# Performance work log

Measured on AMD Instinct MI355X. Metric: run time of the kernel, lower is better.

## Reference

```python
import jax, jax.numpy as jnp
import numpy as np

N_CELLS = 19683   # 27**3 lattice
K = 26            # Moore-neighborhood max_neighbors
D = 128           # state_size
HG = 64           # gating hidden
CNF_STEPS = 3     # integration_steps
DT = 0.1


def setup_inputs() -> dict:
    key = jax.random.key(0)
    ks = jax.random.split(key, 12)
    s = lambda fan_in: 1.0 / np.sqrt(fan_in)
    return {
        "current_state": jax.random.normal(ks[0], (N_CELLS, D), jnp.float32),
        "neighbor_states": jax.random.normal(ks[1], (N_CELLS, K, D), jnp.float32),
        "conn_type": jax.random.randint(ks[2], (N_CELLS, K), 0, 3, jnp.int32),
        "W_local": jax.random.normal(ks[3], (2 * D, D), jnp.float32) * s(2 * D),
        "b_local": jnp.zeros((D,), jnp.float32),
        "W_msg": jax.random.normal(ks[4], (2 * D, D), jnp.float32) * s(2 * D),
        "b_msg": jnp.zeros((D,), jnp.float32),
        "W_upd": jax.random.normal(ks[5], (2 * D, D), jnp.float32) * s(2 * D),
        "b_upd": jnp.zeros((D,), jnp.float32),
        "W_cnf": jax.random.normal(ks[6], (2 * D, D), jnp.float32) * s(2 * D),
        "b_cnf": jnp.zeros((D,), jnp.float32),
        "W_g1": jax.random.normal(ks[7], (D, HG), jnp.float32) * s(D),
        "b_g1": jnp.zeros((HG,), jnp.float32),
        "W_g2": jax.random.normal(ks[8], (HG, 3), jnp.float32) * s(HG),
        "b_g2": jnp.zeros((3,), jnp.float32),
    }


def _masked_mean(nbr, mask):
    # nbr: [N,K,D], mask: [N,K] float -> [N,D]
    cnt = jnp.maximum(mask.sum(-1, keepdims=True), 1.0)
    return jnp.einsum("nkd,nk->nd", nbr, mask) / cnt


def reference(current_state, neighbor_states, conn_type,
              W_local, b_local, W_msg, b_msg, W_upd, b_upd,
              W_cnf, b_cnf, W_g1, b_g1, W_g2, b_g2):
    cur = current_state                       # [N,D]
    nbr = neighbor_states                     # [N,K,D]
    m_l = (conn_type == 0).astype(cur.dtype)  # local mask   [N,K]
    m_f = (conn_type == 1).astype(cur.dtype)  # functional
    m_d = (conn_type == 2).astype(cur.dtype)  # distant

    # --- local expert: SimpleLinear over [cell, mean(local neighbors)] ---
    agg_l = _masked_mean(nbr, m_l)
    local_out = jnp.tanh(jnp.concatenate([cur, agg_l], -1) @ W_local + b_local)

    # --- functional expert: GNN message passing ---
    cur_b = jnp.broadcast_to(cur[:, None, :], nbr.shape)          # [N,K,D]
    edge_in = jnp.concatenate([cur_b, nbr], -1)                   # [N,K,2D]
    msgs = jax.nn.relu(edge_in @ W_msg + b_msg)                   # [N,K,D]
    agg_msg = _masked_mean(msgs, m_f)                             # [N,D]
    func_out = jnp.tanh(jnp.concatenate([cur, agg_msg], -1) @ W_upd + b_upd)

    # --- distant expert: lightweight CNF (fixed-step Euler) ---
    agg_d = _masked_mean(nbr, m_d)

    def euler_step(s, _):
        ds = jnp.tanh(jnp.concatenate([s, agg_d], -1) @ W_cnf + b_cnf)
        return s + DT * ds, None

    distant_out, _ = jax.lax.scan(euler_step, cur, None, length=CNF_STEPS)

    # --- gating network: softmax over 3 experts ---
    gates = jax.nn.softmax(jax.nn.relu(cur @ W_g1 + b_g1) @ W_g2 + b_g2, -1)  # [N,3]

    out = (gates[:, 0:1] * local_out
           + gates[:, 1:2] * func_out
           + gates[:, 2:3] * distant_out)
    return out
```

## Files before the change

### kernel.cpp

```cpp
#include <hip/hip_runtime.h>
#include <hip/hip_bf16.h>
#include <math.h>

#define NC 19683
#define KN 26
#define DD 128
#define HGN 64
#define LDSB 136
#define DTC 0.1f

using bf8v = __attribute__((ext_vector_type(8))) short;
using f4v  = __attribute__((ext_vector_type(4))) float;

__device__ __forceinline__ unsigned short f2bf(float x) {
    union { float f; unsigned u; } v; v.f = x;
    unsigned r = v.u + 0x7fffu + ((v.u >> 16) & 1u);
    return (unsigned short)(r >> 16);
}

__global__ __launch_bounds__(256) void k_prep(const float* __restrict__ Wl,
    const float* __restrict__ Wm, const float* __restrict__ Wu,
    const float* __restrict__ Wc, unsigned short* __restrict__ WT)
{
    int idx = blockIdx.x * 256 + threadIdx.x;
    int m = idx >> 15;
    int r = idx & 32767;
    int j = r >> 8;
    int i = r & 255;
    const float* src = (m == 0) ? Wl : (m == 1) ? Wm : (m == 2) ? Wu : Wc;
    WT[idx] = f2bf(src[i * DD + j]);
}

__global__ __launch_bounds__(256) void kA(const float* __restrict__ cur,
    const unsigned short* __restrict__ WT, const float* __restrict__ b_msg,
    const float* __restrict__ Wg1, const float* __restrict__ bg1,
    const float* __restrict__ Wg2, const float* __restrict__ bg2,
    float* __restrict__ P, float* __restrict__ gates)
{
    __shared__ __align__(16) unsigned short Al[32][LDSB];
    __shared__ __align__(16) unsigned short Bl[128][LDSB];
    __shared__ float curf[32][DD];
    __shared__ float hrelu[32][HGN];
    int t = threadIdx.x;
    int n0 = blockIdx.x * 32;

    for (int p = 0; p < 16; ++p) {
        int idx = p * 256 + t;
        int r = idx >> 7, c = idx & 127;
        float v = (n0 + r < NC) ? cur[(size_t)(n0 + r) * DD + c] : 0.f;
        curf[r][c] = v;
        Al[r][c] = f2bf(v);
    }
    const unsigned short* WmT = WT + 1 * 32768;
    for (int p = 0; p < 8; ++p) {
        int ch = p * 256 + t;
        int j = ch >> 4, i8 = (ch & 15) * 8;
        *(bf8v*)&Bl[j][i8] = *(const bf8v*)&WmT[j * 256 + i8];
    }
    __syncthreads();

    int w = t >> 6, lane = t & 63;
    int mt = w & 1, colh = w >> 1;
    int lm = lane & 15, lq = lane >> 4;
    for (int nt = 0; nt < 4; ++nt) {
        int col0 = colh * 64 + nt * 16;
        f4v acc = {0.f, 0.f, 0.f, 0.f};
        for (int s = 0; s < 4; ++s) {
            bf8v a = *(const bf8v*)&Al[mt * 16 + lm][s * 32 + lq * 8];
            bf8v b = *(const bf8v*)&Bl[col0 + lm][s * 32 + lq * 8];
            acc = __builtin_amdgcn_mfma_f32_16x16x32_bf16(a, b, acc, 0, 0, 0);
        }
        int col = col0 + lm;
        float bm = b_msg[col];
        for (int r = 0; r < 4; ++r) {
            int row = mt * 16 + lq * 4 + r;
            int n = n0 + row;
            if (n < NC) P[(size_t)n * DD + col] = acc[r] + bm;
        }
    }

    for (int p = 0; p < 8; ++p) {
        int idx = p * 256 + t;
        int c = idx >> 6, g = idx & 63;
        float s = bg1[g];
        for (int i = 0; i < DD; ++i) s += curf[c][i] * Wg1[i * HGN + g];
        hrelu[c][g] = fmaxf(s, 0.f);
    }
    __syncthreads();
    if (t < 32) {
        int n = n0 + t;
        if (n < NC) {
            float l[3];
            for (int e = 0; e < 3; ++e) {
                float s = bg2[e];
                for (int g = 0; g < HGN; ++g) s += hrelu[t][g] * Wg2[g * 3 + e];
                l[e] = s;
            }
            float m = fmaxf(l[0], fmaxf(l[1], l[2]));
            float e0 = expf(l[0] - m), e1 = expf(l[1] - m), e2 = expf(l[2] - m);
            float inv = 1.f / (e0 + e1 + e2);
            gates[n * 4 + 0] = e0 * inv;
            gates[n * 4 + 1] = e1 * inv;
            gates[n * 4 + 2] = e2 * inv;
        }
    }
}

__global__ __launch_bounds__(256) void kB(const float* __restrict__ nbr,
    const int* __restrict__ conn, const unsigned short* __restrict__ WT,
    const float* __restrict__ P, float* __restrict__ agg_l,
    float* __restrict__ agg_m, float* __restrict__ agg_d)
{
    __shared__ __align__(16) unsigned short Bl[128][LDSB];
    __shared__ __align__(16) unsigned short Al[2][32][LDSB];
    __shared__ float pbuf[2][DD];
    __shared__ float mlm[2][32], mfm[2][32], mdm[2][32];
    __shared__ float icnt[2][4];
    int t = threadIdx.x;
    int n0 = blockIdx.x * 2;

    if (t < 64) {
        int c = t >> 5, k = t & 31;
        float vl = 0.f, vf = 0.f, vd = 0.f;
        if (k < KN && n0 + c < NC) {
            int ct = conn[(size_t)(n0 + c) * KN + k];
            vl = (ct == 0) ? 1.f : 0.f;
            vf = (ct == 1) ? 1.f : 0.f;
            vd = (ct == 2) ? 1.f : 0.f;
        }
        mlm[c][k] = vl; mfm[c][k] = vf; mdm[c][k] = vd;
    }
    {
        int c = t >> 7, j = t & 127;
        pbuf[c][j] = (n0 + c < NC) ? P[(size_t)(n0 + c) * DD + j] : 0.f;
    }
    const unsigned short* Wm2T = WT + 32768 + 128;
    for (int p = 0; p < 8; ++p) {
        int ch = p * 256 + t;
        int j = ch >> 4, i8 = (ch & 15) * 8;
        *(bf8v*)&Bl[j][i8] = *(const bf8v*)&Wm2T[j * 256 + i8];
    }
    __syncthreads();

    if (t < 2) {
        float cl = 0.f, cf = 0.f, cd = 0.f;
        for (int k = 0; k < KN; ++k) { cl += mlm[t][k]; cf += mfm[t][k]; cd += mdm[t][k]; }
        icnt[t][0] = 1.f / fmaxf(cl, 1.f);
        icnt[t][1] = 1.f / fmaxf(cf, 1.f);
        icnt[t][2] = 1.f / fmaxf(cd, 1.f);
    }

    int c = t >> 7, j = t & 127;
    float sl = 0.f, sd = 0.f;
    if (n0 + c < NC) {
        const float* base = nbr + (size_t)(n0 + c) * KN * DD + j;
        #pragma unroll
        for (int k = 0; k < KN; ++k) {
            float v = base[(size_t)k * DD];
            sl += mlm[c][k] * v;
            sd += mdm[c][k] * v;
            Al[c][k][j] = f2bf(v);
        }
    } else {
        for (int k = 0; k < KN; ++k) Al[c][k][j] = 0;
    }
    for (int k = KN; k < 32; ++k) Al[c][k][j] = 0;
    __syncthreads();

    if (n0 + c < NC) {
        agg_l[(size_t)(n0 + c) * DD + j] = sl * icnt[c][0];
        agg_d[(size_t)(n0 + c) * DD + j] = sd * icnt[c][2];
    }

    int w = t >> 6, lane = t & 63;
    int cc = w >> 1, colh = w & 1;
    int lm = lane & 15, lq = lane >> 4;
    if (n0 + cc < NC) {
        float icf = icnt[cc][1];
        for (int nt = 0; nt < 4; ++nt) {
            int col0 = colh * 64 + nt * 16;
            float pv = pbuf[cc][col0 + lm];
            float msum = 0.f;
            for (int mtile = 0; mtile < 2; ++mtile) {
                f4v acc = {0.f, 0.f, 0.f, 0.f};
                for (int s = 0; s < 4; ++s) {
                    bf8v a = *(const bf8v*)&Al[cc][mtile * 16 + lm][s * 32 + lq * 8];
                    bf8v b = *(const bf8v*)&Bl[col0 + lm][s * 32 + lq * 8];
                    acc = __builtin_amdgcn_mfma_f32_16x16x32_bf16(a, b, acc, 0, 0, 0);
                }
                for (int r = 0; r < 4; ++r) {
                    int row = mtile * 16 + lq * 4 + r;
                    if (mfm[cc][row] > 0.f) msum += fmaxf(pv + acc[r], 0.f);
                }
            }
            msum += __shfl_xor(msum, 16, 64);
            msum += __shfl_xor(msum, 32, 64);
            if (lane < 16) agg_m[(size_t)(n0 + cc) * DD + col0 + lane] = msum * icf;
        }
    }
}

__global__ __launch_bounds__(256) void kC(const float* __restrict__ cur,
    const unsigned short* __restrict__ WT, const float* __restrict__ agg_l,
    const float* __restrict__ agg_m, const float* __restrict__ agg_d,
    const float* __restrict__ b_local, const float* __restrict__ b_upd,
    const float* __restrict__ b_cnf, const float* __restrict__ gates,
    float* __restrict__ out)
{
    __shared__ __align__(16) unsigned short Wl[128][LDSB];
    __shared__ __align__(16) unsigned short Xc[32][LDSB];
    __shared__ __align__(16) unsigned short Xa[32][LDSB];
    __shared__ float glds[32][4];
    __shared__ float bl[DD], bu[DD], bc[DD];
    int t = threadIdx.x;
    int n0 = blockIdx.x * 32;
    int w = t >> 6, lane = t & 63;
    int mt = w & 1, colh = w >> 1;
    int lm = lane & 15, lq = lane >> 4;

    auto stageW = [&](int m, int koff) {
        const unsigned short* src = WT + m * 32768 + koff;
        for (int p = 0; p < 8; ++p) {
            int ch = p * 256 + t;
            int j = ch >> 4, i8 = (ch & 15) * 8;
            *(bf8v*)&Wl[j][i8] = *(const bf8v*)&src[j * 256 + i8];
        }
    };
    auto stageXa = [&](const float* src) {
        for (int p = 0; p < 16; ++p) {
            int idx = p * 256 + t;
            int r = idx >> 7, ccol = idx & 127;
            float v = (n0 + r < NC) ? src[(size_t)(n0 + r) * DD + ccol] : 0.f;
            Xa[r][ccol] = f2bf(v);
        }
    };
    auto mfmaPass = [&](unsigned short (&X)[32][LDSB], f4v* acc) {
        for (int nt = 0; nt < 4; ++nt) {
            int col0 = colh * 64 + nt * 16;
            for (int s = 0; s < 4; ++s) {
                bf8v a = *(const bf8v*)&X[mt * 16 + lm][s * 32 + lq * 8];
                bf8v b = *(const bf8v*)&Wl[col0 + lm][s * 32 + lq * 8];
                acc[nt] = __builtin_amdgcn_mfma_f32_16x16x32_bf16(a, b, acc[nt], 0, 0, 0);
            }
        }
    };

    for (int p = 0; p < 16; ++p) {
        int idx = p * 256 + t;
        int r = idx >> 7, ccol = idx & 127;
        float v = (n0 + r < NC) ? cur[(size_t)(n0 + r) * DD + ccol] : 0.f;
        Xc[r][ccol] = f2bf(v);
    }
    if (t < 128) { bl[t] = b_local[t]; bu[t] = b_upd[t]; bc[t] = b_cnf[t]; }
    if (t >= 128 && t < 160) {
        int r = t - 128; int n = n0 + r;
        float g0 = 0.f, g1 = 0.f, g2 = 0.f;
        if (n < NC) { g0 = gates[n * 4]; g1 = gates[n * 4 + 1]; g2 = gates[n * 4 + 2]; }
        glds[r][0] = g0; glds[r][1] = g1; glds[r][2] = g2;
    }
    stageW(0, 0);
    __syncthreads();

    f4v oacc[4], acc[4];
    for (int nt = 0; nt < 4; ++nt) oacc[nt] = (f4v){0.f, 0.f, 0.f, 0.f};

    for (int nt = 0; nt < 4; ++nt) acc[nt] = (f4v){0.f, 0.f, 0.f, 0.f};
    mfmaPass(Xc, acc);
    __syncthreads();
    stageW(0, 128); stageXa(agg_l);
    __syncthreads();
    mfmaPass(Xa, acc);
    for (int nt = 0; nt < 4; ++nt) {
        int col = colh * 64 + nt * 16 + lm;
        for (int r = 0; r < 4; ++r) {
            int row = mt * 16 + lq * 4 + r;
            oacc[nt][r] += glds[row][0] * tanhf(acc[nt][r] + bl[col]);
        }
    }

    __syncthreads();
    stageW(2, 0);
    __syncthreads();
    for (int nt = 0; nt < 4; ++nt) acc[nt] = (f4v){0.f, 0.f, 0.f, 0.f};
    mfmaPass(Xc, acc);
    __syncthreads();
    stageW(2, 128); stageXa(agg_m);
    __syncthreads();
    mfmaPass(Xa, acc);
    for (int nt = 0; nt < 4; ++nt) {
        int col = colh * 64 + nt * 16 + lm;
        for (int r = 0; r < 4; ++r) {
            int row = mt * 16 + lq * 4 + r;
            oacc[nt][r] += glds[row][1] * tanhf(acc[nt][r] + bu[col]);
        }
    }

    __syncthreads();
    stageW(3, 128); stageXa(agg_d);
    __syncthreads();
    for (int nt = 0; nt < 4; ++nt) acc[nt] = (f4v){0.f, 0.f, 0.f, 0.f};
    mfmaPass(Xa, acc);
    f4v hd[4], s[4];
    for (int nt = 0; nt < 4; ++nt) {
        int col = colh * 64 + nt * 16 + lm;
        for (int r = 0; r < 4; ++r) {
            int row = mt * 16 + lq * 4 + r;
            int n = n0 + row;
            hd[nt][r] = acc[nt][r] + bc[col];
            s[nt][r] = (n < NC) ? cur[(size_t)n * DD + col] : 0.f;
        }
    }
    __syncthreads();
    stageW(3, 0);
    for (int step = 0; step < 3; ++step) {
        for (int nt = 0; nt < 4; ++nt) {
            int col = colh * 64 + nt * 16 + lm;
            for (int r = 0; r < 4; ++r) {
                int row = mt * 16 + lq * 4 + r;
                Xa[row][col] = f2bf(s[nt][r]);
            }
        }
        __syncthreads();
        for (int nt = 0; nt < 4; ++nt) acc[nt] = (f4v){0.f, 0.f, 0.f, 0.f};
        mfmaPass(Xa, acc);
        for (int nt = 0; nt < 4; ++nt)
            for (int r = 0; r < 4; ++r)
                s[nt][r] += DTC * tanhf(acc[nt][r] + hd[nt][r]);
        __syncthreads();
    }

    for (int nt = 0; nt < 4; ++nt) {
        int col = colh * 64 + nt * 16 + lm;
        for (int r = 0; r < 4; ++r) {
            int row = mt * 16 + lq * 4 + r;
            int n = n0 + row;
            if (n < NC) out[(size_t)n * DD + col] = oacc[nt][r] + glds[row][2] * s[nt][r];
        }
    }
}

extern "C" void kernel_launch(void* const* d_in, const int* in_sizes, int n_in,
                              void* d_out, int out_size, void* d_ws, size_t ws_size,
                              hipStream_t stream) {
    const float* cur     = (const float*)d_in[0];
    const float* nbr     = (const float*)d_in[1];
    const int*   conn    = (const int*)d_in[2];
    const float* W_local = (const float*)d_in[3];
    const float* b_local = (const float*)d_in[4];
    const float* W_msg   = (const float*)d_in[5];
    const float* b_msg   = (const float*)d_in[6];
    const float* W_upd   = (const float*)d_in[7];
    const float* b_upd   = (const float*)d_in[8];
    const float* W_cnf   = (const float*)d_in[9];
    const float* b_cnf   = (const float*)d_in[10];
    const float* Wg1     = (const float*)d_in[11];
    const float* bg1     = (const float*)d_in[12];
    const float* Wg2     = (const float*)d_in[13];
    const float* bg2     = (const float*)d_in[14];
    float* out = (float*)d_out;

    char* ws = (char*)d_ws;
    unsigned short* WT = (unsigned short*)ws;
    float* P     = (float*)(ws + 262144);
    float* gatesb = (float*)(ws + 262144 + 10077696);
    float* aggl  = (float*)(ws + 262144 + 10077696 + 314928);
    float* aggm  = aggl + (size_t)NC * DD;
    float* aggd  = aggm + (size_t)NC * DD;

    hipLaunchKernelGGL(k_prep, dim3(512), dim3(256), 0, stream, W_local, W_msg, W_upd, W_cnf, WT);
    hipLaunchKernelGGL(kA, dim3(616), dim3(256), 0, stream, cur, WT, b_msg, Wg1, bg1, Wg2, bg2, P, gatesb);
    hipLaunchKernelGGL(kB, dim3(9842), dim3(256), 0, stream, nbr, conn, WT, P, aggl, aggm, aggd);
    hipLaunchKernelGGL(kC, dim3(616), dim3(256), 0, stream, cur, WT, aggl, aggm, aggd, b_local, b_upd, b_cnf, gatesb, out);
}
```

Measured before the change: 544.2 us.

## Restructure neighbor kernel per-wave, store aggregates as bf16, MFMA gating

The neighbor kernel now assigns one cell per wave (four cells per block). It builds the connection-type masks with wave ballots and popcounts instead of shared-memory arrays, and uses float2 vector loads for the neighbor rows. The three aggregate buffers are written as bf16 instead of fp32, which halves the intermediate traffic between the neighbor kernel and the final kernel, and the final kernel reads them with 16-byte vector loads. The gating first layer moves from a scalar fp32 loop to bf16 MFMA using a pre-transposed weight, which gives up some precision in the gates and the aggregates.

```diff
diff --git a/kernel.cpp b/kernel.cpp
--- a/kernel.cpp
+++ b/kernel.cpp
@@ -17,74 +17,98 @@
     unsigned r = v.u + 0x7fffu + ((v.u >> 16) & 1u);
     return (unsigned short)(r >> 16);
 }
+__device__ __forceinline__ unsigned pk2(float a, float b) {
+    return ((unsigned)f2bf(a)) | (((unsigned)f2bf(b)) << 16);
+}
 
 __global__ __launch_bounds__(256) void k_prep(const float* __restrict__ Wl,
     const float* __restrict__ Wm, const float* __restrict__ Wu,
-    const float* __restrict__ Wc, unsigned short* __restrict__ WT)
+    const float* __restrict__ Wc, const float* __restrict__ Wg1,
+    unsigned short* __restrict__ WT, unsigned short* __restrict__ WgT)
 {
     int idx = blockIdx.x * 256 + threadIdx.x;
-    int m = idx >> 15;
-    int r = idx & 32767;
-    int j = r >> 8;
-    int i = r & 255;
-    const float* src = (m == 0) ? Wl : (m == 1) ? Wm : (m == 2) ? Wu : Wc;
-    WT[idx] = f2bf(src[i * DD + j]);
+    if (idx < 131072) {
+        int m = idx >> 15;
+        int r = idx & 32767;
+        int j = r >> 8;
+        int i = r & 255;
+        const float* src = (m == 0) ? Wl : (m == 1) ? Wm : (m == 2) ? Wu : Wc;
+        WT[idx] = f2bf(src[i * DD + j]);
+    } else {
+        int idx2 = idx - 131072;
+        int col = idx2 >> 7;
+        int k = idx2 & 127;
+        WgT[idx2] = f2bf(Wg1[k * HGN + col]);
+    }
 }
 
 __global__ __launch_bounds__(256) void kA(const float* __restrict__ cur,
-    const unsigned short* __restrict__ WT, const float* __restrict__ b_msg,
-    const float* __restrict__ Wg1, const float* __restrict__ bg1,
+    const unsigned short* __restrict__ WT, const unsigned short* __restrict__ WgT,
+    const float* __restrict__ b_msg, const float* __restrict__ bg1,
     const float* __restrict__ Wg2, const float* __restrict__ bg2,
     float* __restrict__ P, float* __restrict__ gates)
 {
     __shared__ __align__(16) unsigned short Al[32][LDSB];
     __shared__ __align__(16) unsigned short Bl[128][LDSB];
-    __shared__ float curf[32][DD];
-    __shared__ float hrelu[32][HGN];
+    __shared__ __align__(16) unsigned short Gl[64][LDSB];
+    __shared__ float hrelu[32][HGN + 4];
     int t = threadIdx.x;
     int n0 = blockIdx.x * 32;
-
-    for (int p = 0; p < 16; ++p) {
+    int w = t >> 6, lane = t & 63;
+    int lm = lane & 15, lq = lane >> 4;
+
+    for (int p = 0; p < 8; ++p) {
         int idx = p * 256 + t;
-        int r = idx >> 7, c = idx & 127;
-        float v = (n0 + r < NC) ? cur[(size_t)(n0 + r) * DD + c] : 0.f;
-        curf[r][c] = v;
-        Al[r][c] = f2bf(v);
-    }
-    const unsigned short* WmT = WT + 1 * 32768;
+        int r = idx >> 6, c2 = (idx & 63) * 2;
+        float2 v = {0.f, 0.f};
+        if (n0 + r < NC) v = *(const float2*)&cur[(size_t)(n0 + r) * DD + c2];
+        *(unsigned*)&Al[r][c2] = pk2(v.x, v.y);
+    }
+    const unsigned short* WmT = WT + 32768;
     for (int p = 0; p < 8; ++p) {
         int ch = p * 256 + t;
         int j = ch >> 4, i8 = (ch & 15) * 8;
         *(bf8v*)&Bl[j][i8] = *(const bf8v*)&WmT[j * 256 + i8];
     }
-    __syncthreads();
-
-    int w = t >> 6, lane = t & 63;
-    int mt = w & 1, colh = w >> 1;
-    int lm = lane & 15, lq = lane >> 4;
-    for (int nt = 0; nt < 4; ++nt) {
-        int col0 = colh * 64 + nt * 16;
-        f4v acc = {0.f, 0.f, 0.f, 0.f};
-        for (int s = 0; s < 4; ++s) {
-            bf8v a = *(const bf8v*)&Al[mt * 16 + lm][s * 32 + lq * 8];
-            bf8v b = *(const bf8v*)&Bl[col0 + lm][s * 32 + lq * 8];
-            acc = __builtin_amdgcn_mfma_f32_16x16x32_bf16(a, b, acc, 0, 0, 0);
-        }
-        int col = col0 + lm;
-        float bm = b_msg[col];
-        for (int r = 0; r < 4; ++r) {
-            int row = mt * 16 + lq * 4 + r;
-            int n = n0 + row;
-            if (n < NC) P[(size_t)n * DD + col] = acc[r] + bm;
-        }
-    }
-
-    for (int p = 0; p < 8; ++p) {
-        int idx = p * 256 + t;
-        int c = idx >> 6, g = idx & 63;
-        float s = bg1[g];
-        for (int i = 0; i < DD; ++i) s += curf[c][i] * Wg1[i * HGN + g];
-        hrelu[c][g] = fmaxf(s, 0.f);
+    for (int p = 0; p < 4; ++p) {
+        int ch = p * 256 + t;
+        int j = ch >> 4, i8 = (ch & 15) * 8;
+        *(bf8v*)&Gl[j][i8] = *(const bf8v*)&WgT[j * 128 + i8];
+    }
+    __syncthreads();
+
+    {
+        int mt = w & 1, colh = w >> 1;
+        for (int nt = 0; nt < 4; ++nt) {
+            int col0 = colh * 64 + nt * 16;
+            f4v acc = {0.f, 0.f, 0.f, 0.f};
+            for (int s = 0; s < 4; ++s) {
+                bf8v a = *(const bf8v*)&Al[mt * 16 + lm][s * 32 + lq * 8];
+                bf8v b = *(const bf8v*)&Bl[col0 + lm][s * 32 + lq * 8];
+                acc = __builtin_amdgcn_mfma_f32_16x16x32_bf16(a, b, acc, 0, 0, 0);
+            }
+            int col = col0 + lm;
+            float bm = b_msg[col];
+            for (int r = 0; r < 4; ++r) {
+                int row = mt * 16 + lq * 4 + r;
+                int n = n0 + row;
+                if (n < NC) P[(size_t)n * DD + col] = acc[r] + bm;
+            }
+        }
+    }
+    {
+        int col0 = w * 16;
+        float bg = bg1[col0 + lm];
+        for (int mt2 = 0; mt2 < 2; ++mt2) {
+            f4v acc = {0.f, 0.f, 0.f, 0.f};
+            for (int s = 0; s < 4; ++s) {
+                bf8v a = *(const bf8v*)&Al[mt2 * 16 + lm][s * 32 + lq * 8];
+                bf8v b = *(const bf8v*)&Gl[col0 + lm][s * 32 + lq * 8];
+                acc = __builtin_amdgcn_mfma_f32_16x16x32_bf16(a, b, acc, 0, 0, 0);
+            }
+            for (int r = 0; r < 4; ++r)
+                hrelu[mt2 * 16 + lq * 4 + r][col0 + lm] = fmaxf(acc[r] + bg, 0.f);
+        }
     }
     __syncthreads();
     if (t < 32) {
@@ -108,101 +132,95 @@
 
 __global__ __launch_bounds__(256) void kB(const float* __restrict__ nbr,
     const int* __restrict__ conn, const unsigned short* __restrict__ WT,
-    const float* __restrict__ P, float* __restrict__ agg_l,
-    float* __restrict__ agg_m, float* __restrict__ agg_d)
+    const float* __restrict__ P, unsigned short* __restrict__ agg_l,
+    unsigned short* __restrict__ agg_m, unsigned short* __restrict__ agg_d)
 {
     __shared__ __align__(16) unsigned short Bl[128][LDSB];
-    __shared__ __align__(16) unsigned short Al[2][32][LDSB];
-    __shared__ float pbuf[2][DD];
-    __shared__ float mlm[2][32], mfm[2][32], mdm[2][32];
-    __shared__ float icnt[2][4];
+    __shared__ __align__(16) unsigned short Al[4][32][LDSB];
+    __shared__ float P8[4][DD];
     int t = threadIdx.x;
-    int n0 = blockIdx.x * 2;
-
-    if (t < 64) {
-        int c = t >> 5, k = t & 31;
-        float vl = 0.f, vf = 0.f, vd = 0.f;
-        if (k < KN && n0 + c < NC) {
-            int ct = conn[(size_t)(n0 + c) * KN + k];
-            vl = (ct == 0) ? 1.f : 0.f;
-            vf = (ct == 1) ? 1.f : 0.f;
-            vd = (ct == 2) ? 1.f : 0.f;
-        }
-        mlm[c][k] = vl; mfm[c][k] = vf; mdm[c][k] = vd;
-    }
-    {
-        int c = t >> 7, j = t & 127;
-        pbuf[c][j] = (n0 + c < NC) ? P[(size_t)(n0 + c) * DD + j] : 0.f;
-    }
+    int n0 = blockIdx.x * 4;
+    int w = t >> 6, lane = t & 63;
+    int n = n0 + w;
+    bool act = n < NC;
+
     const unsigned short* Wm2T = WT + 32768 + 128;
     for (int p = 0; p < 8; ++p) {
         int ch = p * 256 + t;
         int j = ch >> 4, i8 = (ch & 15) * 8;
         *(bf8v*)&Bl[j][i8] = *(const bf8v*)&Wm2T[j * 256 + i8];
     }
-    __syncthreads();
-
-    if (t < 2) {
-        float cl = 0.f, cf = 0.f, cd = 0.f;
-        for (int k = 0; k < KN; ++k) { cl += mlm[t][k]; cf += mfm[t][k]; cd += mdm[t][k]; }
-        icnt[t][0] = 1.f / fmaxf(cl, 1.f);
-        icnt[t][1] = 1.f / fmaxf(cf, 1.f);
-        icnt[t][2] = 1.f / fmaxf(cd, 1.f);
-    }
-
-    int c = t >> 7, j = t & 127;
-    float sl = 0.f, sd = 0.f;
-    if (n0 + c < NC) {
-        const float* base = nbr + (size_t)(n0 + c) * KN * DD + j;
-        #pragma unroll
-        for (int k = 0; k < KN; ++k) {
-            float v = base[(size_t)k * DD];
-            sl += mlm[c][k] * v;
-            sd += mdm[c][k] * v;
-            Al[c][k][j] = f2bf(v);
-        }
-    } else {
-        for (int k = 0; k < KN; ++k) Al[c][k][j] = 0;
-    }
-    for (int k = KN; k < 32; ++k) Al[c][k][j] = 0;
-    __syncthreads();
-
-    if (n0 + c < NC) {
-        agg_l[(size_t)(n0 + c) * DD + j] = sl * icnt[c][0];
-        agg_d[(size_t)(n0 + c) * DD + j] = sd * icnt[c][2];
-    }
-
-    int w = t >> 6, lane = t & 63;
-    int cc = w >> 1, colh = w & 1;
-    int lm = lane & 15, lq = lane >> 4;
-    if (n0 + cc < NC) {
-        float icf = icnt[cc][1];
-        for (int nt = 0; nt < 4; ++nt) {
-            int col0 = colh * 64 + nt * 16;
-            float pv = pbuf[cc][col0 + lm];
+    {
+        int idx = t * 2;
+        int r = idx >> 7, c = idx & 127;
+        float2 v = {0.f, 0.f};
+        if (n0 + r < NC) v = *(const float2*)&P[(size_t)(n0 + r) * DD + c];
+        *(float2*)&P8[r][c] = v;
+    }
+    int ct = 3;
+    if (act && lane < KN) ct = conn[(size_t)n * KN + lane];
+    unsigned long long mlb = __ballot(ct == 0);
+    unsigned long long mfb = __ballot(ct == 1);
+    unsigned long long mdb = __ballot(ct == 2);
+    float icl = 1.f / fmaxf((float)__builtin_popcountll(mlb), 1.f);
+    float icf = 1.f / fmaxf((float)__builtin_popcountll(mfb), 1.f);
+    float icd = 1.f / fmaxf((float)__builtin_popcountll(mdb), 1.f);
+
+    int j2 = lane * 2;
+    const float* base = nbr + ((size_t)(act ? n : 0) * KN) * DD + j2;
+    float2 vv[KN];
+    #pragma unroll
+    for (int k = 0; k < KN; ++k) {
+        float2 v = {0.f, 0.f};
+        if (act) v = *(const float2*)&base[(size_t)k * DD];
+        vv[k] = v;
+    }
+    float slx = 0.f, sly = 0.f, sdx = 0.f, sdy = 0.f;
+    #pragma unroll
+    for (int k = 0; k < KN; ++k) {
+        float2 v = vv[k];
+        if ((mlb >> k) & 1) { slx += v.x; sly += v.y; }
+        if ((mdb >> k) & 1) { sdx += v.x; sdy += v.y; }
+        *(unsigned*)&Al[w][k][j2] = pk2(v.x, v.y);
+    }
+    {
+        unsigned* pz = (unsigned*)&Al[w][KN][0];
+        for (int z = lane; z < (32 - KN) * LDSB / 2; z += 64) pz[z] = 0;
+    }
+    if (act) {
+        *(unsigned*)&agg_l[(size_t)n * DD + j2] = pk2(slx * icl, sly * icl);
+        *(unsigned*)&agg_d[(size_t)n * DD + j2] = pk2(sdx * icd, sdy * icd);
+    }
+    __syncthreads();
+
+    if (act) {
+        int lm = lane & 15, lq = lane >> 4;
+        for (int nt = 0; nt < 8; ++nt) {
+            int col0 = nt * 16;
+            float pv = P8[w][col0 + lm];
             float msum = 0.f;
-            for (int mtile = 0; mtile < 2; ++mtile) {
+            for (int mt2 = 0; mt2 < 2; ++mt2) {
                 f4v acc = {0.f, 0.f, 0.f, 0.f};
                 for (int s = 0; s < 4; ++s) {
-                    bf8v a = *(const bf8v*)&Al[cc][mtile * 16 + lm][s * 32 + lq * 8];
+                    bf8v a = *(const bf8v*)&Al[w][mt2 * 16 + lm][s * 32 + lq * 8];
                     bf8v b = *(const bf8v*)&Bl[col0 + lm][s * 32 + lq * 8];
                     acc = __builtin_amdgcn_mfma_f32_16x16x32_bf16(a, b, acc, 0, 0, 0);
                 }
                 for (int r = 0; r < 4; ++r) {
-                    int row = mtile * 16 + lq * 4 + r;
-                    if (mfm[cc][row] > 0.f) msum += fmaxf(pv + acc[r], 0.f);
+                    int row = mt2 * 16 + lq * 4 + r;
+                    if ((mfb >> row) & 1) msum += fmaxf(pv + acc[r], 0.f);
                 }
             }
             msum += __shfl_xor(msum, 16, 64);
             msum += __shfl_xor(msum, 32, 64);
-            if (lane < 16) agg_m[(size_t)(n0 + cc) * DD + col0 + lane] = msum * icf;
+            if (lane < 16) agg_m[(size_t)n * DD + col0 + lane] = f2bf(msum * icf);
         }
     }
 }
 
 __global__ __launch_bounds__(256) void kC(const float* __restrict__ cur,
-    const unsigned short* __restrict__ WT, const float* __restrict__ agg_l,
-    const float* __restrict__ agg_m, const float* __restrict__ agg_d,
+    const unsigned short* __restrict__ WT, const unsigned short* __restrict__ agg_l,
+    const unsigned short* __restrict__ agg_m, const unsigned short* __restrict__ agg_d,
     const float* __restrict__ b_local, const float* __restrict__ b_upd,
     const float* __restrict__ b_cnf, const float* __restrict__ gates,
     float* __restrict__ out)
@@ -226,12 +244,13 @@
             *(bf8v*)&Wl[j][i8] = *(const bf8v*)&src[j * 256 + i8];
         }
     };
-    auto stageXa = [&](const float* src) {
-        for (int p = 0; p < 16; ++p) {
+    auto stageXa = [&](const unsigned short* src) {
+        for (int p = 0; p < 2; ++p) {
             int idx = p * 256 + t;
-            int r = idx >> 7, ccol = idx & 127;
-            float v = (n0 + r < NC) ? src[(size_t)(n0 + r) * DD + ccol] : 0.f;
-            Xa[r][ccol] = f2bf(v);
+            int r = idx >> 4, c8 = (idx & 15) * 8;
+            bf8v v = {0, 0, 0, 0, 0, 0, 0, 0};
+            if (n0 + r < NC) v = *(const bf8v*)&src[(size_t)(n0 + r) * DD + c8];
+            *(bf8v*)&Xa[r][c8] = v;
         }
     };
     auto mfmaPass = [&](unsigned short (&X)[32][LDSB], f4v* acc) {
@@ -245,11 +264,12 @@
         }
     };
 
-    for (int p = 0; p < 16; ++p) {
+    for (int p = 0; p < 8; ++p) {
         int idx = p * 256 + t;
-        int r = idx >> 7, ccol = idx & 127;
-        float v = (n0 + r < NC) ? cur[(size_t)(n0 + r) * DD + ccol] : 0.f;
-        Xc[r][ccol] = f2bf(v);
+        int r = idx >> 6, c2 = (idx & 63) * 2;
+        float2 v = {0.f, 0.f};
+        if (n0 + r < NC) v = *(const float2*)&cur[(size_t)(n0 + r) * DD + c2];
+        *(unsigned*)&Xc[r][c2] = pk2(v.x, v.y);
     }
     if (t < 128) { bl[t] = b_local[t]; bu[t] = b_upd[t]; bc[t] = b_cnf[t]; }
     if (t >= 128 && t < 160) {
@@ -360,15 +380,16 @@
     float* out = (float*)d_out;
 
     char* ws = (char*)d_ws;
-    unsigned short* WT = (unsigned short*)ws;
-    float* P     = (float*)(ws + 262144);
-    float* gatesb = (float*)(ws + 262144 + 10077696);
-    float* aggl  = (float*)(ws + 262144 + 10077696 + 314928);
-    float* aggm  = aggl + (size_t)NC * DD;
-    float* aggd  = aggm + (size_t)NC * DD;
-
-    hipLaunchKernelGGL(k_prep, dim3(512), dim3(256), 0, stream, W_local, W_msg, W_upd, W_cnf, WT);
-    hipLaunchKernelGGL(kA, dim3(616), dim3(256), 0, stream, cur, WT, b_msg, Wg1, bg1, Wg2, bg2, P, gatesb);
-    hipLaunchKernelGGL(kB, dim3(9842), dim3(256), 0, stream, nbr, conn, WT, P, aggl, aggm, aggd);
+    unsigned short* WT  = (unsigned short*)ws;
+    unsigned short* WgT = (unsigned short*)(ws + 262144);
+    float* P      = (float*)(ws + 278528);
+    float* gatesb = (float*)(ws + 278528 + 10077696);
+    unsigned short* aggl = (unsigned short*)(ws + 278528 + 10077696 + 314928);
+    unsigned short* aggm = aggl + (size_t)NC * DD;
+    unsigned short* aggd = aggm + (size_t)NC * DD;
+
+    hipLaunchKernelGGL(k_prep, dim3(544), dim3(256), 0, stream, W_local, W_msg, W_upd, W_cnf, Wg1, WT, WgT);
+    hipLaunchKernelGGL(kA, dim3(616), dim3(256), 0, stream, cur, WT, WgT, b_msg, bg1, Wg2, bg2, P, gatesb);
+    hipLaunchKernelGGL(kB, dim3(4921), dim3(256), 0, stream, nbr, conn, WT, P, aggl, aggm, aggd);
     hipLaunchKernelGGL(kC, dim3(616), dim3(256), 0, stream, cur, WT, aggl, aggm, aggd, b_local, b_upd, b_cnf, gatesb, out);
 }
```

After: 457.8 us. 1.19x faster.
